# Performance work log

Hardware: AMD Instinct MI355X
Metric: run time of the kernel (lower is better)

Reference implementation:

```python
import jax, jax.numpy as jnp
import numpy as np

N_NODES = 100000
FEAT = 256      # input_size == out_size (required for multi-layer consistency in original code)
OUT = 256
B = 20000       # batch of target nodes
S = 25          # sampled neighbors per node (padded)


def setup_inputs() -> dict:
    key = jax.random.key(0)
    k1, k2, k3, k4, k5, k6 = jax.random.split(key, 6)
    feats = jax.random.normal(k1, (N_NODES, FEAT), dtype=jnp.float32)
    nodes = jax.random.randint(k2, (B,), 0, N_NODES)
    samp_neighs = jax.random.randint(k3, (B, S), 0, N_NODES)
    val_lens = jax.random.randint(k4, (B,), 1, S + 1)  # at least 1 valid neighbor
    # xavier_uniform-like scale for [out, 2*in] weights
    s0 = (6.0 / (OUT + 2 * FEAT)) ** 0.5
    s1 = (6.0 / (OUT + 2 * OUT)) ** 0.5
    w0 = jax.random.uniform(k5, (OUT, 2 * FEAT), jnp.float32, -s0, s0)
    w1 = jax.random.uniform(k6, (OUT, 2 * OUT), jnp.float32, -s1, s1)
    return {"feats": feats, "nodes": nodes, "samp_neighs": samp_neighs,
            "val_lens": val_lens, "w0": w0, "w1": w1}


def _mean_agg(neigh_feats, val_lens):
    # neigh_feats: [B, S, F]; ragged MEAN over first val_lens[b] neighbors
    mask = (jnp.arange(neigh_feats.shape[1])[None, :] < val_lens[:, None]).astype(neigh_feats.dtype)
    summed = jnp.einsum('bsf,bs->bf', neigh_feats, mask)
    return summed / val_lens[:, None].astype(neigh_feats.dtype)


def reference(feats, nodes, samp_neighs, val_lens, w0, w1):
    self_raw = feats[nodes]           # [B, F] gather
    neigh = feats[samp_neighs]        # [B, S, F] gather
    agg = _mean_agg(neigh, val_lens)  # [B, F]
    feat_data = self_raw
    for w in (w0, w1):
        # SageLayer: relu(W @ concat(self, agg).T).T == relu(concat @ W.T)
        combined = jnp.concatenate([self_raw, agg], axis=1)  # [B, 2F]
        feat_data = jax.nn.relu(combined @ w.T)              # [B, OUT]
        # Original recomputes aggregator with feat_data as self_feats, but MEAN
        # aggregation (gcn=False) depends only on raw neighbor feats -> identical.
        agg = _mean_agg(neigh, val_lens)
    return feat_data
```

## Files before the change

kernel.cpp:

```cpp
#include <hip/hip_runtime.h>

typedef unsigned short u16;
typedef unsigned int   u32;

#define NB     20000
#define SNB    25
#define FEAT   256
#define K2     512
#define OUTF   256

#define WS_W1_OFF (NB * K2 * 2)

__device__ __forceinline__ u32 f2bf(float f) {
  union { u32 i; float f; } x; x.f = f;
  return (x.i + 0x7fffu + ((x.i >> 16) & 1u)) >> 16;
}
__device__ __forceinline__ u32 pack2(float a, float b) {
  return f2bf(a) | (f2bf(b) << 16);
}

__global__ __launch_bounds__(256) void convw_kernel(
    const float* __restrict__ w_raw, u16* __restrict__ w_bf) {
  const int i = blockIdx.x * 256 + threadIdx.x;
  w_bf[i] = (u16)f2bf(w_raw[i]);
}

__global__ __launch_bounds__(256) void agg_kernel(
    const float* __restrict__ feats, const int* __restrict__ nodes,
    const int* __restrict__ neighs, const int* __restrict__ lens,
    u16* __restrict__ combined) {
  const int b    = blockIdx.x * 4 + (threadIdx.x >> 6);
  const int lane = threadIdx.x & 63;

  const int self = nodes[b];
  const int len  = lens[b];
  int myidx = (lane < SNB) ? neighs[b * SNB + lane] : 0;

  const float4 sv = ((const float4*)(feats + (size_t)self * FEAT))[lane];

  float4 a0 = {0.f, 0.f, 0.f, 0.f}, a1 = a0, a2 = a0, a3 = a0;
  int s = 0;
  for (; s + 4 <= len; s += 4) {
    const int i0 = __shfl(myidx, s);
    const int i1 = __shfl(myidx, s + 1);
    const int i2 = __shfl(myidx, s + 2);
    const int i3 = __shfl(myidx, s + 3);
    const float4 v0 = ((const float4*)(feats + (size_t)i0 * FEAT))[lane];
    const float4 v1 = ((const float4*)(feats + (size_t)i1 * FEAT))[lane];
    const float4 v2 = ((const float4*)(feats + (size_t)i2 * FEAT))[lane];
    const float4 v3 = ((const float4*)(feats + (size_t)i3 * FEAT))[lane];
    a0.x += v0.x; a0.y += v0.y; a0.z += v0.z; a0.w += v0.w;
    a1.x += v1.x; a1.y += v1.y; a1.z += v1.z; a1.w += v1.w;
    a2.x += v2.x; a2.y += v2.y; a2.z += v2.z; a2.w += v2.w;
    a3.x += v3.x; a3.y += v3.y; a3.z += v3.z; a3.w += v3.w;
  }
  for (; s < len; ++s) {
    const int i0 = __shfl(myidx, s);
    const float4 v0 = ((const float4*)(feats + (size_t)i0 * FEAT))[lane];
    a0.x += v0.x; a0.y += v0.y; a0.z += v0.z; a0.w += v0.w;
  }
  const float inv = 1.f / (float)len;
  const float m0 = (a0.x + a1.x + a2.x + a3.x) * inv;
  const float m1 = (a0.y + a1.y + a2.y + a3.y) * inv;
  const float m2 = (a0.z + a1.z + a2.z + a3.z) * inv;
  const float m3 = (a0.w + a1.w + a2.w + a3.w) * inv;

  uint2* crow = (uint2*)(combined + (size_t)b * K2);
  uint2 pe; pe.x = pack2(sv.x, sv.y); pe.y = pack2(sv.z, sv.w);
  crow[lane] = pe;
  uint2 pm; pm.x = pack2(m0, m1); pm.y = pack2(m2, m3);
  crow[64 + lane] = pm;
}

typedef __attribute__((ext_vector_type(8))) short short8;
typedef __attribute__((ext_vector_type(4))) float f32x4;

#define BM 128
#define BN 128
#define BK 32
#define LDST 40

__global__ __launch_bounds__(256) void gemm_kernel(
    const u16* __restrict__ A,
    const u16* __restrict__ W,
    float* __restrict__ C,
    int M) {
  __shared__ u16 As[BM * LDST];
  __shared__ u16 Bs[BN * LDST];

  const int tid  = threadIdx.x;
  const int wave = tid >> 6;
  const int lane = tid & 63;
  const int m0 = blockIdx.x * BM;
  const int n0 = blockIdx.y * BN;

  const int wr = (wave >> 1) * 64;
  const int wc = (wave & 1) * 64;

  f32x4 acc[4][4] = {};

  const int r16 = lane & 15;
  const int kq  = (lane >> 4) * 8;

  const int srow = tid >> 2;
  const int skc  = tid & 3;

  for (int k0 = 0; k0 < K2; k0 += BK) {
#pragma unroll
    for (int i = 0; i < 2; ++i) {
      const int row = i * 64 + srow;
      int ar = m0 + row; if (ar >= M) ar = M - 1;
      const uint4 va = ((const uint4*)(A + (size_t)ar * K2 + k0))[skc];
      *(uint4*)&As[row * LDST + skc * 8] = va;
      const uint4 vb = ((const uint4*)(W + (size_t)(n0 + row) * K2 + k0))[skc];
      *(uint4*)&Bs[row * LDST + skc * 8] = vb;
    }
    __syncthreads();

    short8 af[4], bf[4];
#pragma unroll
    for (int i = 0; i < 4; ++i)
      af[i] = *(const short8*)&As[(wr + i * 16 + r16) * LDST + kq];
#pragma unroll
    for (int j = 0; j < 4; ++j)
      bf[j] = *(const short8*)&Bs[(wc + j * 16 + r16) * LDST + kq];

#pragma unroll
    for (int i = 0; i < 4; ++i)
#pragma unroll
      for (int j = 0; j < 4; ++j)
        acc[i][j] = __builtin_amdgcn_mfma_f32_16x16x32_bf16(af[i], bf[j],
                                                            acc[i][j], 0, 0, 0);
    __syncthreads();
  }

#pragma unroll
  for (int i = 0; i < 4; ++i) {
#pragma unroll
    for (int r = 0; r < 4; ++r) {
      const int row = m0 + wr + i * 16 + (lane >> 4) * 4 + r;
      if (row < M) {
#pragma unroll
        for (int j = 0; j < 4; ++j) {
          const int col = n0 + wc + j * 16 + (lane & 15);
          float v = acc[i][j][r];
          C[(size_t)row * OUTF + col] = v > 0.f ? v : 0.f;
        }
      }
    }
  }
}

extern "C" void kernel_launch(void* const* d_in, const int* in_sizes, int n_in,
                              void* d_out, int out_size, void* d_ws, size_t ws_size,
                              hipStream_t stream) {
  const float* feats = (const float*)d_in[0];
  const int* nodes   = (const int*)d_in[1];
  const int* neighs  = (const int*)d_in[2];
  const int* lens    = (const int*)d_in[3];
  const float* w1    = (const float*)d_in[5];
  float* out = (float*)d_out;

  char* ws = (char*)d_ws;
  u16* combined = (u16*)ws;
  u16* w1bf     = (u16*)(ws + WS_W1_OFF);

  convw_kernel<<<512, 256, 0, stream>>>(w1, w1bf);
  agg_kernel<<<NB / 4, 256, 0, stream>>>(feats, nodes, neighs, lens, combined);

  dim3 grid((NB + BM - 1) / BM, OUTF / BN);
  gemm_kernel<<<grid, 256, 0, stream>>>(combined, w1bf, out, NB);
}
```

Measured before the change: 199.7 us.

## Fuse neighbor aggregation and GEMM into one kernel via shared-memory A tile

Merges the gather/mean aggregation kernel and the bf16 MFMA GEMM into one kernel. Each block aggregates 32 rows straight into LDS and multiplies them against the whole 256-wide weight matrix, streamed in K chunks. This removes the global write and re-read of the 20000x512 bf16 combined buffer and one launch. In exchange each block has only 32 rows, so every block reloads all of W, and the gather and MFMA phases are serialized within a block with no overlap between them.

New measurement: 205.7 us. +3.0%, slower.

```diff
diff --git a/kernel.cpp b/kernel.cpp
--- a/kernel.cpp
+++ b/kernel.cpp
@@ -9,7 +9,15 @@
 #define K2     512
 #define OUTF   256
 
-#define WS_W1_OFF (NB * K2 * 2)
+#define BM     32
+#define NPW    8
+#define LDA    520
+#define BK     32
+#define LDB    40
+#define NCHUNK (K2 / BK)
+
+typedef __attribute__((ext_vector_type(8))) short short8;
+typedef __attribute__((ext_vector_type(4))) float f32x4;
 
 __device__ __forceinline__ u32 f2bf(float f) {
   union { u32 i; float f; } x; x.f = f;
@@ -25,130 +33,114 @@
   w_bf[i] = (u16)f2bf(w_raw[i]);
 }
 
-__global__ __launch_bounds__(256) void agg_kernel(
+__global__ __launch_bounds__(256) void fused_kernel(
     const float* __restrict__ feats, const int* __restrict__ nodes,
     const int* __restrict__ neighs, const int* __restrict__ lens,
-    u16* __restrict__ combined) {
-  const int b    = blockIdx.x * 4 + (threadIdx.x >> 6);
-  const int lane = threadIdx.x & 63;
+    const u16* __restrict__ W, float* __restrict__ C) {
+  __shared__ u16 As[BM * LDA];
+  __shared__ u16 Bs[OUTF * LDB];
 
-  const int self = nodes[b];
-  const int len  = lens[b];
-  int myidx = (lane < SNB) ? neighs[b * SNB + lane] : 0;
+  const int tid   = threadIdx.x;
+  const int wave  = tid >> 6;
+  const int lane  = tid & 63;
+  const int mbase = blockIdx.x * BM;
 
-  const float4 sv = ((const float4*)(feats + (size_t)self * FEAT))[lane];
+  {
+    const uint4* src = (const uint4*)(W + (size_t)tid * K2);
+    uint4* dst = (uint4*)&Bs[tid * LDB];
+#pragma unroll
+    for (int c = 0; c < 4; ++c) dst[c] = src[c];
+  }
 
-  float4 a0 = {0.f, 0.f, 0.f, 0.f}, a1 = a0, a2 = a0, a3 = a0;
-  int s = 0;
-  for (; s + 4 <= len; s += 4) {
-    const int i0 = __shfl(myidx, s);
-    const int i1 = __shfl(myidx, s + 1);
-    const int i2 = __shfl(myidx, s + 2);
-    const int i3 = __shfl(myidx, s + 3);
-    const float4 v0 = ((const float4*)(feats + (size_t)i0 * FEAT))[lane];
-    const float4 v1 = ((const float4*)(feats + (size_t)i1 * FEAT))[lane];
-    const float4 v2 = ((const float4*)(feats + (size_t)i2 * FEAT))[lane];
-    const float4 v3 = ((const float4*)(feats + (size_t)i3 * FEAT))[lane];
-    a0.x += v0.x; a0.y += v0.y; a0.z += v0.z; a0.w += v0.w;
-    a1.x += v1.x; a1.y += v1.y; a1.z += v1.z; a1.w += v1.w;
-    a2.x += v2.x; a2.y += v2.y; a2.z += v2.z; a2.w += v2.w;
-    a3.x += v3.x; a3.y += v3.y; a3.z += v3.z; a3.w += v3.w;
+  for (int p = 0; p < NPW; ++p) {
+    const int m = wave * NPW + p;
+    const int b = mbase + m;
+    const int self = nodes[b];
+    const int len  = lens[b];
+    int myidx = (lane < SNB) ? neighs[b * SNB + lane] : 0;
+
+    const float4 sv = ((const float4*)(feats + (size_t)self * FEAT))[lane];
+
+    float4 a0 = {0.f, 0.f, 0.f, 0.f}, a1 = a0, a2 = a0, a3 = a0;
+    int s = 0;
+    for (; s + 4 <= len; s += 4) {
+      const int i0 = __shfl(myidx, s);
+      const int i1 = __shfl(myidx, s + 1);
+      const int i2 = __shfl(myidx, s + 2);
+      const int i3 = __shfl(myidx, s + 3);
+      const float4 v0 = ((const float4*)(feats + (size_t)i0 * FEAT))[lane];
+      const float4 v1 = ((const float4*)(feats + (size_t)i1 * FEAT))[lane];
+      const float4 v2 = ((const float4*)(feats + (size_t)i2 * FEAT))[lane];
+      const float4 v3 = ((const float4*)(feats + (size_t)i3 * FEAT))[lane];
+      a0.x += v0.x; a0.y += v0.y; a0.z += v0.z; a0.w += v0.w;
+      a1.x += v1.x; a1.y += v1.y; a1.z += v1.z; a1.w += v1.w;
+      a2.x += v2.x; a2.y += v2.y; a2.z += v2.z; a2.w += v2.w;
+      a3.x += v3.x; a3.y += v3.y; a3.z += v3.z; a3.w += v3.w;
+    }
+    for (; s < len; ++s) {
+      const int i0 = __shfl(myidx, s);
+      const float4 v0 = ((const float4*)(feats + (size_t)i0 * FEAT))[lane];
+      a0.x += v0.x; a0.y += v0.y; a0.z += v0.z; a0.w += v0.w;
+    }
+    const float inv = 1.f / (float)len;
+    const float m0 = (a0.x + a1.x + a2.x + a3.x) * inv;
+    const float m1 = (a0.y + a1.y + a2.y + a3.y) * inv;
+    const float m2 = (a0.z + a1.z + a2.z + a3.z) * inv;
+    const float m3 = (a0.w + a1.w + a2.w + a3.w) * inv;
+
+    uint2* arow = (uint2*)&As[m * LDA];
+    uint2 pe; pe.x = pack2(sv.x, sv.y); pe.y = pack2(sv.z, sv.w);
+    arow[lane] = pe;
+    uint2 pm; pm.x = pack2(m0, m1); pm.y = pack2(m2, m3);
+    arow[64 + lane] = pm;
   }
-  for (; s < len; ++s) {
-    const int i0 = __shfl(myidx, s);
-    const float4 v0 = ((const float4*)(feats + (size_t)i0 * FEAT))[lane];
-    a0.x += v0.x; a0.y += v0.y; a0.z += v0.z; a0.w += v0.w;
-  }
-  const float inv = 1.f / (float)len;
-  const float m0 = (a0.x + a1.x + a2.x + a3.x) * inv;
-  const float m1 = (a0.y + a1.y + a2.y + a3.y) * inv;
-  const float m2 = (a0.z + a1.z + a2.z + a3.z) * inv;
-  const float m3 = (a0.w + a1.w + a2.w + a3.w) * inv;
+  __syncthreads();
 
-  uint2* crow = (uint2*)(combined + (size_t)b * K2);
-  uint2 pe; pe.x = pack2(sv.x, sv.y); pe.y = pack2(sv.z, sv.w);
-  crow[lane] = pe;
-  uint2 pm; pm.x = pack2(m0, m1); pm.y = pack2(m2, m3);
-  crow[64 + lane] = pm;
-}
-
-typedef __attribute__((ext_vector_type(8))) short short8;
-typedef __attribute__((ext_vector_type(4))) float f32x4;
-
-#define BM 128
-#define BN 128
-#define BK 32
-#define LDST 40
-
-__global__ __launch_bounds__(256) void gemm_kernel(
-    const u16* __restrict__ A,
-    const u16* __restrict__ W,
-    float* __restrict__ C,
-    int M) {
-  __shared__ u16 As[BM * LDST];
-  __shared__ u16 Bs[BN * LDST];
-
-  const int tid  = threadIdx.x;
-  const int wave = tid >> 6;
-  const int lane = tid & 63;
-  const int m0 = blockIdx.x * BM;
-  const int n0 = blockIdx.y * BN;
-
-  const int wr = (wave >> 1) * 64;
-  const int wc = (wave & 1) * 64;
-
-  f32x4 acc[4][4] = {};
-
+  const int wc  = wave * 64;
   const int r16 = lane & 15;
   const int kq  = (lane >> 4) * 8;
 
-  const int srow = tid >> 2;
-  const int skc  = tid & 3;
+  f32x4 acc[2][4] = {};
 
-  for (int k0 = 0; k0 < K2; k0 += BK) {
+  for (int kc = 0; ; ) {
+    const int k0 = kc * BK;
+    short8 af[2], bf[4];
 #pragma unroll
-    for (int i = 0; i < 2; ++i) {
-      const int row = i * 64 + srow;
-      int ar = m0 + row; if (ar >= M) ar = M - 1;
-      const uint4 va = ((const uint4*)(A + (size_t)ar * K2 + k0))[skc];
-      *(uint4*)&As[row * LDST + skc * 8] = va;
-      const uint4 vb = ((const uint4*)(W + (size_t)(n0 + row) * K2 + k0))[skc];
-      *(uint4*)&Bs[row * LDST + skc * 8] = vb;
-    }
-    __syncthreads();
-
-    short8 af[4], bf[4];
-#pragma unroll
-    for (int i = 0; i < 4; ++i)
-      af[i] = *(const short8*)&As[(wr + i * 16 + r16) * LDST + kq];
+    for (int i = 0; i < 2; ++i)
+      af[i] = *(const short8*)&As[(i * 16 + r16) * LDA + k0 + kq];
 #pragma unroll
     for (int j = 0; j < 4; ++j)
-      bf[j] = *(const short8*)&Bs[(wc + j * 16 + r16) * LDST + kq];
+      bf[j] = *(const short8*)&Bs[(wc + j * 16 + r16) * LDB + kq];
 
 #pragma unroll
-    for (int i = 0; i < 4; ++i)
+    for (int i = 0; i < 2; ++i)
 #pragma unroll
       for (int j = 0; j < 4; ++j)
         acc[i][j] = __builtin_amdgcn_mfma_f32_16x16x32_bf16(af[i], bf[j],
                                                             acc[i][j], 0, 0, 0);
+    if (++kc == NCHUNK) break;
+    __syncthreads();
+    {
+      const uint4* src = (const uint4*)(W + (size_t)tid * K2 + kc * BK);
+      uint4* dst = (uint4*)&Bs[tid * LDB];
+#pragma unroll
+      for (int c = 0; c < 4; ++c) dst[c] = src[c];
+    }
     __syncthreads();
   }
 
 #pragma unroll
-  for (int i = 0; i < 4; ++i) {
+  for (int i = 0; i < 2; ++i)
 #pragma unroll
     for (int r = 0; r < 4; ++r) {
-      const int row = m0 + wr + i * 16 + (lane >> 4) * 4 + r;
-      if (row < M) {
+      const int row = mbase + i * 16 + (lane >> 4) * 4 + r;
 #pragma unroll
-        for (int j = 0; j < 4; ++j) {
-          const int col = n0 + wc + j * 16 + (lane & 15);
-          float v = acc[i][j][r];
-          C[(size_t)row * OUTF + col] = v > 0.f ? v : 0.f;
-        }
+      for (int j = 0; j < 4; ++j) {
+        const int col = wc + j * 16 + (lane & 15);
+        const float v = acc[i][j][r];
+        C[(size_t)row * OUTF + col] = v > 0.f ? v : 0.f;
       }
     }
-  }
 }
 
 extern "C" void kernel_launch(void* const* d_in, const int* in_sizes, int n_in,
@@ -161,13 +153,8 @@
   const float* w1    = (const float*)d_in[5];
   float* out = (float*)d_out;
 
-  char* ws = (char*)d_ws;
-  u16* combined = (u16*)ws;
-  u16* w1bf     = (u16*)(ws + WS_W1_OFF);
+  u16* w1bf = (u16*)d_ws;
 
   convw_kernel<<<512, 256, 0, stream>>>(w1, w1bf);
-  agg_kernel<<<NB / 4, 256, 0, stream>>>(feats, nodes, neighs, lens, combined);
-
-  dim3 grid((NB + BM - 1) / BM, OUTF / BN);
-  gemm_kernel<<<grid, 256, 0, stream>>>(combined, w1bf, out, NB);
+  fused_kernel<<<NB / BM, 256, 0, stream>>>(feats, nodes, neighs, lens, w1bf, out);
 }
```

## Project all node features through weights before gathering and averaging neighbors

Applied to the files above, without the earlier changes.

Uses the linearity of the mean to push the weight multiply before aggregation. A GEMM projects every node's features through both weight halves into a bf16 table. A final kernel then gathers the projected self row and the neighbor rows, averages them, adds and applies ReLU. This halves the bytes per neighbor gather (bf16 of 256 outputs instead of fp32 of 256 features), at the cost of a GEMM over all 100k nodes, a large workspace and extra bf16 rounding. The old path stays as a fallback when the workspace is too small.

Result: slower. 252.6 us (+26.5%).

```diff
diff --git a/kernel.cpp b/kernel.cpp
--- a/kernel.cpp
+++ b/kernel.cpp
@@ -8,8 +8,18 @@
 #define FEAT   256
 #define K2     512
 #define OUTF   256
-
-#define WS_W1_OFF (NB * K2 * 2)
+#define NNODES 100000
+
+#define WS_T_BYTES   (NNODES * K2 * 2)
+#define WS_WT_OFF    WS_T_BYTES
+#define WS_WT_BYTES  (K2 * FEAT * 2)
+#define WS_NEED      (WS_WT_OFF + WS_WT_BYTES)
+
+#define WSF_W1_OFF   (NB * K2 * 2)
+#define WSF_NEED     (WSF_W1_OFF + WS_WT_BYTES)
+
+typedef __attribute__((ext_vector_type(8))) short short8;
+typedef __attribute__((ext_vector_type(4))) float f32x4;
 
 __device__ __forceinline__ u32 f2bf(float f) {
   union { u32 i; float f; } x; x.f = f;
@@ -18,26 +28,188 @@
 __device__ __forceinline__ u32 pack2(float a, float b) {
   return f2bf(a) | (f2bf(b) << 16);
 }
-
-__global__ __launch_bounds__(256) void convw_kernel(
+__device__ __forceinline__ float4 unbf4(uint2 u) {
+  float4 r;
+  r.x = __uint_as_float(u.x << 16);
+  r.y = __uint_as_float(u.x & 0xffff0000u);
+  r.z = __uint_as_float(u.y << 16);
+  r.w = __uint_as_float(u.y & 0xffff0000u);
+  return r;
+}
+
+__global__ __launch_bounds__(256) void convwt_kernel(
+    const float* __restrict__ w1, u16* __restrict__ wt) {
+  const int idx = blockIdx.x * 256 + threadIdx.x;
+  const int j = idx >> 8;
+  const int k = idx & 255;
+  const float v = (j < 256) ? w1[j * K2 + k] : w1[(j - 256) * K2 + 256 + k];
+  wt[idx] = (u16)f2bf(v);
+}
+
+#define TM   128
+#define TBK  32
+#define LDST 40
+
+__global__ __launch_bounds__(256) void tgemm_kernel(
+    const float* __restrict__ feats,
+    const u16* __restrict__ Wt,
+    u16* __restrict__ T) {
+  __shared__ u16 As[TM * LDST];
+  __shared__ u16 Bs[TM * LDST];
+
+  const int tid  = threadIdx.x;
+  const int wave = tid >> 6;
+  const int lane = tid & 63;
+  const int m0 = blockIdx.x * TM;
+  const int n0 = blockIdx.y * TM;
+
+  const int wr = (wave >> 1) * 64;
+  const int wc = (wave & 1) * 64;
+
+  f32x4 acc[4][4] = {};
+
+  const int r16 = lane & 15;
+  const int kq  = (lane >> 4) * 8;
+
+  const int sr = tid >> 1;
+  const int sh = tid & 1;
+
+  for (int k0 = 0; k0 < FEAT; k0 += TBK) {
+    {
+      int ar = m0 + sr; if (ar >= NNODES) ar = NNODES - 1;
+      const float4* src = (const float4*)(feats + (size_t)ar * FEAT + k0 + sh * 16);
+      const float4 f0 = src[0], f1 = src[1], f2 = src[2], f3 = src[3];
+      uint4 o0, o1;
+      o0.x = pack2(f0.x, f0.y); o0.y = pack2(f0.z, f0.w);
+      o0.z = pack2(f1.x, f1.y); o0.w = pack2(f1.z, f1.w);
+      o1.x = pack2(f2.x, f2.y); o1.y = pack2(f2.z, f2.w);
+      o1.z = pack2(f3.x, f3.y); o1.w = pack2(f3.z, f3.w);
+      *(uint4*)&As[sr * LDST + sh * 16]     = o0;
+      *(uint4*)&As[sr * LDST + sh * 16 + 8] = o1;
+    }
+    {
+      const uint4* src = (const uint4*)(Wt + (size_t)(n0 + sr) * FEAT + k0 + sh * 16);
+      *(uint4*)&Bs[sr * LDST + sh * 16]     = src[0];
+      *(uint4*)&Bs[sr * LDST + sh * 16 + 8] = src[1];
+    }
+    __syncthreads();
+
+    short8 af[4], bf[4];
+#pragma unroll
+    for (int i = 0; i < 4; ++i)
+      af[i] = *(const short8*)&As[(wr + i * 16 + r16) * LDST + kq];
+#pragma unroll
+    for (int j = 0; j < 4; ++j)
+      bf[j] = *(const short8*)&Bs[(wc + j * 16 + r16) * LDST + kq];
+
+#pragma unroll
+    for (int i = 0; i < 4; ++i)
+#pragma unroll
+      for (int j = 0; j < 4; ++j)
+        acc[i][j] = __builtin_amdgcn_mfma_f32_16x16x32_bf16(af[i], bf[j],
+                                                            acc[i][j], 0, 0, 0);
+    __syncthreads();
+  }
+
+#pragma unroll
+  for (int i = 0; i < 4; ++i) {
+#pragma unroll
+    for (int r = 0; r < 4; ++r) {
+      const int row = m0 + wr + i * 16 + (lane >> 4) * 4 + r;
+      if (row < NNODES) {
+#pragma unroll
+        for (int j = 0; j < 4; ++j) {
+          const int col = n0 + wc + j * 16 + r16;
+          T[(size_t)row * K2 + col] = (u16)f2bf(acc[i][j][r]);
+        }
+      }
+    }
+  }
+}
+
+__global__ __launch_bounds__(256) void final_kernel(
+    const u16* __restrict__ T, const int* __restrict__ nodes,
+    const int* __restrict__ neighs, const int* __restrict__ lens,
+    float* __restrict__ C) {
+  const int b    = blockIdx.x * 4 + (threadIdx.x >> 6);
+  const int lane = threadIdx.x & 63;
+
+  const int self = nodes[b];
+  const int len  = lens[b];
+  int myidx = (lane < SNB) ? neighs[b * SNB + lane] : 0;
+
+  const uint2 sp = *(const uint2*)(T + (size_t)self * K2 + lane * 4);
+  const float4 p = unbf4(sp);
+
+  float4 a0 = {0.f, 0.f, 0.f, 0.f}, a1 = a0, a2 = a0, a3 = a0;
+  float4 a4 = a0, a5 = a0, a6 = a0, a7 = a0;
+  int s = 0;
+  for (; s + 8 <= len; s += 8) {
+    const int i0 = __shfl(myidx, s);
+    const int i1 = __shfl(myidx, s + 1);
+    const int i2 = __shfl(myidx, s + 2);
+    const int i3 = __shfl(myidx, s + 3);
+    const int i4 = __shfl(myidx, s + 4);
+    const int i5 = __shfl(myidx, s + 5);
+    const int i6 = __shfl(myidx, s + 6);
+    const int i7 = __shfl(myidx, s + 7);
+    const uint2 q0 = *(const uint2*)(T + (size_t)i0 * K2 + 256 + lane * 4);
+    const uint2 q1 = *(const uint2*)(T + (size_t)i1 * K2 + 256 + lane * 4);
+    const uint2 q2 = *(const uint2*)(T + (size_t)i2 * K2 + 256 + lane * 4);
+    const uint2 q3 = *(const uint2*)(T + (size_t)i3 * K2 + 256 + lane * 4);
+    const uint2 q4 = *(const uint2*)(T + (size_t)i4 * K2 + 256 + lane * 4);
+    const uint2 q5 = *(const uint2*)(T + (size_t)i5 * K2 + 256 + lane * 4);
+    const uint2 q6 = *(const uint2*)(T + (size_t)i6 * K2 + 256 + lane * 4);
+    const uint2 q7 = *(const uint2*)(T + (size_t)i7 * K2 + 256 + lane * 4);
+    float4 v;
+    v = unbf4(q0); a0.x += v.x; a0.y += v.y; a0.z += v.z; a0.w += v.w;
+    v = unbf4(q1); a1.x += v.x; a1.y += v.y; a1.z += v.z; a1.w += v.w;
+    v = unbf4(q2); a2.x += v.x; a2.y += v.y; a2.z += v.z; a2.w += v.w;
+    v = unbf4(q3); a3.x += v.x; a3.y += v.y; a3.z += v.z; a3.w += v.w;
+    v = unbf4(q4); a4.x += v.x; a4.y += v.y; a4.z += v.z; a4.w += v.w;
+    v = unbf4(q5); a5.x += v.x; a5.y += v.y; a5.z += v.z; a5.w += v.w;
+    v = unbf4(q6); a6.x += v.x; a6.y += v.y; a6.z += v.z; a6.w += v.w;
+    v = unbf4(q7); a7.x += v.x; a7.y += v.y; a7.z += v.z; a7.w += v.w;
+  }
+  for (; s < len; ++s) {
+    const int i0 = __shfl(myidx, s);
+    const uint2 q0 = *(const uint2*)(T + (size_t)i0 * K2 + 256 + lane * 4);
+    const float4 v = unbf4(q0);
+    a0.x += v.x; a0.y += v.y; a0.z += v.z; a0.w += v.w;
+  }
+  a0.x += a4.x; a0.y += a4.y; a0.z += a4.z; a0.w += a4.w;
+  a1.x += a5.x; a1.y += a5.y; a1.z += a5.z; a1.w += a5.w;
+  a2.x += a6.x; a2.y += a6.y; a2.z += a6.z; a2.w += a6.w;
+  a3.x += a7.x; a3.y += a7.y; a3.z += a7.z; a3.w += a7.w;
+  const float inv = 1.f / (float)len;
+  float4 o;
+  o.x = p.x + (a0.x + a1.x + a2.x + a3.x) * inv;
+  o.y = p.y + (a0.y + a1.y + a2.y + a3.y) * inv;
+  o.z = p.z + (a0.z + a1.z + a2.z + a3.z) * inv;
+  o.w = p.w + (a0.w + a1.w + a2.w + a3.w) * inv;
+  o.x = o.x > 0.f ? o.x : 0.f;
+  o.y = o.y > 0.f ? o.y : 0.f;
+  o.z = o.z > 0.f ? o.z : 0.f;
+  o.w = o.w > 0.f ? o.w : 0.f;
+  ((float4*)(C + (size_t)b * OUTF))[lane] = o;
+}
+
+__global__ __launch_bounds__(256) void convw_fb_kernel(
     const float* __restrict__ w_raw, u16* __restrict__ w_bf) {
   const int i = blockIdx.x * 256 + threadIdx.x;
   w_bf[i] = (u16)f2bf(w_raw[i]);
 }
 
-__global__ __launch_bounds__(256) void agg_kernel(
+__global__ __launch_bounds__(256) void agg_fb_kernel(
     const float* __restrict__ feats, const int* __restrict__ nodes,
     const int* __restrict__ neighs, const int* __restrict__ lens,
     u16* __restrict__ combined) {
   const int b    = blockIdx.x * 4 + (threadIdx.x >> 6);
   const int lane = threadIdx.x & 63;
-
   const int self = nodes[b];
   const int len  = lens[b];
   int myidx = (lane < SNB) ? neighs[b * SNB + lane] : 0;
-
   const float4 sv = ((const float4*)(feats + (size_t)self * FEAT))[lane];
-
   float4 a0 = {0.f, 0.f, 0.f, 0.f}, a1 = a0, a2 = a0, a3 = a0;
   int s = 0;
   for (; s + 4 <= len; s += 4) {
@@ -64,7 +236,6 @@
   const float m1 = (a0.y + a1.y + a2.y + a3.y) * inv;
   const float m2 = (a0.z + a1.z + a2.z + a3.z) * inv;
   const float m3 = (a0.w + a1.w + a2.w + a3.w) * inv;
-
   uint2* crow = (uint2*)(combined + (size_t)b * K2);
   uint2 pe; pe.x = pack2(sv.x, sv.y); pe.y = pack2(sv.z, sv.w);
   crow[lane] = pe;
@@ -72,40 +243,24 @@
   crow[64 + lane] = pm;
 }
 
-typedef __attribute__((ext_vector_type(8))) short short8;
-typedef __attribute__((ext_vector_type(4))) float f32x4;
-
-#define BM 128
-#define BN 128
-#define BK 32
-#define LDST 40
-
-__global__ __launch_bounds__(256) void gemm_kernel(
-    const u16* __restrict__ A,
-    const u16* __restrict__ W,
-    float* __restrict__ C,
-    int M) {
-  __shared__ u16 As[BM * LDST];
-  __shared__ u16 Bs[BN * LDST];
-
+__global__ __launch_bounds__(256) void gemm_fb_kernel(
+    const u16* __restrict__ A, const u16* __restrict__ W,
+    float* __restrict__ C, int M) {
+  __shared__ u16 As[128 * LDST];
+  __shared__ u16 Bs[128 * LDST];
   const int tid  = threadIdx.x;
   const int wave = tid >> 6;
   const int lane = tid & 63;
-  const int m0 = blockIdx.x * BM;
-  const int n0 = blockIdx.y * BN;
-
+  const int m0 = blockIdx.x * 128;
+  const int n0 = blockIdx.y * 128;
   const int wr = (wave >> 1) * 64;
   const int wc = (wave & 1) * 64;
-
   f32x4 acc[4][4] = {};
-
   const int r16 = lane & 15;
   const int kq  = (lane >> 4) * 8;
-
   const int srow = tid >> 2;
   const int skc  = tid & 3;
-
-  for (int k0 = 0; k0 < K2; k0 += BK) {
+  for (int k0 = 0; k0 < K2; k0 += 32) {
 #pragma unroll
     for (int i = 0; i < 2; ++i) {
       const int row = i * 64 + srow;
@@ -116,7 +271,6 @@
       *(uint4*)&Bs[row * LDST + skc * 8] = vb;
     }
     __syncthreads();
-
     short8 af[4], bf[4];
 #pragma unroll
     for (int i = 0; i < 4; ++i)
@@ -124,7 +278,6 @@
 #pragma unroll
     for (int j = 0; j < 4; ++j)
       bf[j] = *(const short8*)&Bs[(wc + j * 16 + r16) * LDST + kq];
-
 #pragma unroll
     for (int i = 0; i < 4; ++i)
 #pragma unroll
@@ -133,7 +286,6 @@
                                                             acc[i][j], 0, 0, 0);
     __syncthreads();
   }
-
 #pragma unroll
   for (int i = 0; i < 4; ++i) {
 #pragma unroll
@@ -162,12 +314,21 @@
   float* out = (float*)d_out;
 
   char* ws = (char*)d_ws;
-  u16* combined = (u16*)ws;
-  u16* w1bf     = (u16*)(ws + WS_W1_OFF);
-
-  convw_kernel<<<512, 256, 0, stream>>>(w1, w1bf);
-  agg_kernel<<<NB / 4, 256, 0, stream>>>(feats, nodes, neighs, lens, combined);
-
-  dim3 grid((NB + BM - 1) / BM, OUTF / BN);
-  gemm_kernel<<<grid, 256, 0, stream>>>(combined, w1bf, out, NB);
-}
+
+  if (ws_size >= (size_t)WS_NEED) {
+    u16* T  = (u16*)ws;
+    u16* Wt = (u16*)(ws + WS_WT_OFF);
+
+    convwt_kernel<<<512, 256, 0, stream>>>(w1, Wt);
+    dim3 tg((NNODES + TM - 1) / TM, K2 / TM);
+    tgemm_kernel<<<tg, 256, 0, stream>>>(feats, Wt, T);
+    final_kernel<<<NB / 4, 256, 0, stream>>>(T, nodes, neighs, lens, out);
+  } else {
+    u16* combined = (u16*)ws;
+    u16* w1bf     = (u16*)(ws + WSF_W1_OFF);
+    convw_fb_kernel<<<512, 256, 0, stream>>>(w1, w1bf);
+    agg_fb_kernel<<<NB / 4, 256, 0, stream>>>(feats, nodes, neighs, lens, combined);
+    dim3 grid((NB + 127) / 128, OUTF / 128);
+    gemm_fb_kernel<<<grid, 256, 0, stream>>>(combined, w1bf, out, NB);
+  }
+}
```
